# Performance work log

Hardware: AMD Instinct MI355X
Metric: run time of the kernel (lower is better)

## Reference

```python
import jax, jax.numpy as jnp
import numpy as np

KS = 16
FREQ = jnp.array([0., 1., 2., 4., 8., 16., 32., 64.], dtype=jnp.float32)  # [0]+[2^i], d=8
TWO_PI = 2.0 * np.pi


def softplus_b10(x):
    # torch F.softplus(x, beta=10, threshold=1): linear when beta*x > threshold
    bx = 10.0 * x
    return jnp.where(bx > 1.0, x, jnp.log1p(jnp.exp(jnp.minimum(bx, 1.0))) / 10.0)


def grid_sample_2d(img, gx, gy):
    # img: (C, H, W) complex; gx,gy: (N,) in [-1,1]. Bilinear, align_corners=True,
    # zero padding -- matches torch.nn.functional.grid_sample. Returns (C, N).
    C, H, W = img.shape
    ix = (gx + 1.0) * 0.5 * (W - 1)
    iy = (gy + 1.0) * 0.5 * (H - 1)
    ix0 = jnp.floor(ix)
    iy0 = jnp.floor(iy)
    wx = ix - ix0
    wy = iy - iy0

    def corner(iyc, ixc, w):
        valid = (ixc >= 0) & (ixc <= W - 1) & (iyc >= 0) & (iyc <= H - 1)
        ii = jnp.clip(ixc, 0, W - 1).astype(jnp.int32)
        jj = jnp.clip(iyc, 0, H - 1).astype(jnp.int32)
        return img[:, jj, ii] * (w * valid)[None, :]

    return (corner(iy0, ix0, (1 - wx) * (1 - wy))
            + corner(iy0, ix0 + 1, wx * (1 - wy))
            + corner(iy0 + 1, ix0, (1 - wx) * wy)
            + corner(iy0 + 1, ix0 + 1, wx * wy))


def batch_irfft(P, x):
    # P: (ks, d, N) complex; x: (N,) in [-1,1]. Trig-weighted inverse rFFT reduce.
    xx = (x + 1.0) * 0.5
    ang = TWO_PI * xx[:, None] * FREQ[None, :]            # (N, d)
    scale = jnp.where(FREQ > 0, 2.0, 1.0)
    c = jnp.cos(ang) * scale
    s = jnp.sin(ang) * scale
    return jnp.einsum('kdn,nd->kn', P.real, c) - jnp.einsum('kdn,nd->kn', P.imag, s)


def reference(xyz, bound, alpha_params, Pu_re, Pu_im, Pv_re, Pv_im, Pw_re, Pw_im):
    alpha = softplus_b10(alpha_params)[0]
    Pu = jnp.fft.ifftn((Pu_re + 1j * Pu_im) * alpha, axes=(3, 4))  # (1,ks,dx,Ny,Nz)
    Pv = jnp.fft.ifftn((Pv_re + 1j * Pv_im) * alpha, axes=(2, 4))  # (1,ks,Nx,dy,Nz)
    Pw = jnp.fft.ifftn((Pw_re + 1j * Pw_im) * alpha, axes=(2, 3))  # (1,ks,Nx,Ny,dz)

    xyzn = xyz / bound
    xs, ys, zs = xyzn[:, 0], xyzn[:, 1], xyzn[:, 2]
    N = xs.shape[0]

    ks, dx = Pu.shape[1], Pu.shape[2]
    dy = Pv.shape[3]
    dz = Pw.shape[4]

    # Pu: sample over (Ny, Nz) plane; grid (x=zs -> width Nz, y=ys -> height Ny)
    Px = grid_sample_2d(Pu[0].reshape(ks * dx, Pu.shape[3], Pu.shape[4]), zs, ys).reshape(ks, dx, N)
    # Pv: transpose (ks,Nx,dy,Nz)->(ks,dy,Nx,Nz); grid (x=zs -> Nz, y=xs -> Nx)
    Py = grid_sample_2d(jnp.swapaxes(Pv[0], 1, 2).reshape(ks * dy, Pv.shape[2], Pv.shape[4]), zs, xs).reshape(ks, dy, N)
    # Pw: transpose (ks,Nx,Ny,dz)->(ks,dz,Ny,Nx); grid (x=xs -> Nx, y=ys -> Ny)
    Pz = grid_sample_2d(jnp.swapaxes(Pw[0], 1, 3).reshape(ks * dz, Pw.shape[3], Pw.shape[2]), xs, ys).reshape(ks, dz, N)

    P = batch_irfft(Px, xs) + batch_irfft(Py, ys) + batch_irfft(Pz, zs)  # (ks, N)
    return P.T  # (N, ks)


def setup_inputs() -> dict:
    key = jax.random.key(0)
    ks = jax.random.split(key, 8)
    N = 131072
    xyz = jax.random.uniform(ks[0], (N, 3), dtype=jnp.float32, minval=-1.0, maxval=1.0)
    scale = 0.05
    return {
        'xyz': xyz,
        'bound': 1.0,
        'alpha_params': jnp.full((1,), 0.001, dtype=jnp.float32),
        'Pu_re': scale * jax.random.normal(ks[1], (1, KS, 8, 160, 160), dtype=jnp.float32),
        'Pu_im': scale * jax.random.normal(ks[2], (1, KS, 8, 160, 160), dtype=jnp.float32),
        'Pv_re': scale * jax.random.normal(ks[3], (1, KS, 160, 8, 160), dtype=jnp.float32),
        'Pv_im': scale * jax.random.normal(ks[4], (1, KS, 160, 8, 160), dtype=jnp.float32),
        'Pw_re': scale * jax.random.normal(ks[5], (1, KS, 160, 160, 8), dtype=jnp.float32),
        'Pw_im': scale * jax.random.normal(ks[6], (1, KS, 160, 160, 8), dtype=jnp.float32),
    }
```

## Files before the change

### kernel.cpp

```cpp
#include <hip/hip_runtime.h>
#include <hip/hip_bf16.h>

#define G 160
#define GM1 159
#define KD 128
#define KP 320
#define PLANE_U 3276800
#define NBUCK 4096
#define TWO_PI_F 6.28318530717958647692f

#define TSCALE 256.0f
#define TSCALE_INV 0.00390625f

typedef __attribute__((ext_vector_type(8))) short bf16x8;
typedef __attribute__((ext_vector_type(4))) float f32x4;
typedef _Float16 half2t __attribute__((ext_vector_type(2)));
typedef __fp16 fp16x2 __attribute__((ext_vector_type(2)));

__device__ __forceinline__ unsigned short f2bf(float x) {
    unsigned u = __float_as_uint(x);
    unsigned r = (u + 0x7FFFu + ((u >> 16) & 1u)) >> 16;
    return (unsigned short)r;
}
__device__ __forceinline__ unsigned int packbf(float re, float im) {
    union { __hip_bfloat162 h; unsigned int u; } cv;
    cv.h = __float22bfloat162_rn(make_float2(re, im));
    return cv.u;
}
__device__ __forceinline__ half2t cvtpk(float a, float b) {
    union { fp16x2 f; half2t h; } cv;
    cv.f = __builtin_amdgcn_cvt_pkrtz(a, b);
    return cv.h;
}
__device__ __forceinline__ unsigned int packh(float re, float im) {
    union { fp16x2 f; unsigned int u; } cv;
    cv.f = __builtin_amdgcn_cvt_pkrtz(re, im);
    return cv.u;
}
__device__ __forceinline__ half2t u2h2(unsigned int u) {
    union { unsigned int u; half2t h; } cv;
    cv.u = u;
    return cv.h;
}
__device__ __forceinline__ float fdot2h(half2t a, half2t b, float acc) {
#if __has_builtin(__builtin_amdgcn_fdot2)
    return __builtin_amdgcn_fdot2(a, b, acc, false);
#else
    return acc + (float)a.x * (float)b.x + (float)a.y * (float)b.y;
#endif
}
__device__ __forceinline__ unsigned int wim_of(unsigned int u) {
    return ((u << 16) | (u >> 16)) ^ 0x00008000u;
}
__device__ __forceinline__ unsigned part1by2(unsigned x) {
    x &= 0x3FF;
    x = (x | (x << 16)) & 0xFF0000FFu;
    x = (x | (x << 8))  & 0x0300F00Fu;
    x = (x | (x << 4))  & 0x030C30C3u;
    x = (x | (x << 2))  & 0x09249249u;
    return x;
}
__device__ __forceinline__ unsigned morton_key(float x, float y, float z) {
    int cx = min(max((int)((x + 1.0f) * 8.0f), 0), 15);
    int cy = min(max((int)((y + 1.0f) * 8.0f), 0), 15);
    int cz = min(max((int)((z + 1.0f) * 8.0f), 0), 15);
    return part1by2(cx) | (part1by2(cy) << 1) | (part1by2(cz) << 2);
}

__global__ __launch_bounds__(256) void k_prep(
    const float* __restrict__ Pw_re, const float* __restrict__ Pw_im,
    unsigned int* __restrict__ Apw, unsigned short* __restrict__ Wre,
    unsigned int* __restrict__ counts)
{
    __shared__ unsigned int sT[64 * 33];
    int b = blockIdx.x;
    int tid = threadIdx.x;
    if (b < 16) {
        counts[b * 256 + tid] = 0;
        return;
    }
    if (b < 216) {
        int idx = (b - 16) * 256 + tid;
        int r = idx / KP, kp = idx - r * KP;
        int q = kp >> 1;
        int m = (r * q) % G;
        float th = (float)m * (TWO_PI_F / (float)G);
        float s, c;
        __sincosf(th, &s, &c);
        Wre[idx] = f2bf(((kp & 1) == 0 ? c : -s) * (1.0f / (float)G));
        return;
    }
    int b2 = b - 216;
    int k  = b2 / 100;
    int rem = b2 - k * 100;
    int pc = rem / 5;
    int q0 = (rem - pc * 5) * 32;

    int i = tid & 63, qo = tid >> 6;
    size_t base = (size_t)k * 204800 + (size_t)pc * 64 + i;
    #pragma unroll
    for (int qc = 0; qc < 8; qc++) {
        int q = q0 + qo * 8 + qc;
        float r  = Pw_re[base + (size_t)q * 1280];
        float im = Pw_im[base + (size_t)q * 1280];
        sT[i * 33 + qo * 8 + qc] = packbf(r, im);
    }
    __syncthreads();
    int qp = tid & 31, mo = tid >> 5;
    #pragma unroll
    for (int mc = 0; mc < 8; mc++) {
        int m = (k * 8 + mo) * G + pc * 8 + mc;
        Apw[(size_t)m * G + q0 + qp] = sT[(mc * 8 + mo) * 33 + qp];
    }
}

__global__ __launch_bounds__(256) void k_hist(
    const float* __restrict__ xyz, const float* __restrict__ bound,
    unsigned int* __restrict__ counts, int N)
{
    int i = blockIdx.x * blockDim.x + threadIdx.x;
    if (i >= N) return;
    float invb = 1.0f / bound[0];
    float x = xyz[3 * i + 0] * invb;
    float y = xyz[3 * i + 1] * invb;
    float z = xyz[3 * i + 2] * invb;
    atomicAdd(&counts[morton_key(x, y, z)], 1u);
}

__global__ __launch_bounds__(1024) void k_scan(
    const unsigned int* __restrict__ counts,
    unsigned int* __restrict__ cursors)
{
    __shared__ unsigned int ws[16];
    int t = threadIdx.x;
    int lane = t & 63, wid = t >> 6;
    unsigned int local[4];
    unsigned int s = 0;
    #pragma unroll
    for (int i = 0; i < 4; i++) { local[i] = counts[t * 4 + i]; s += local[i]; }
    unsigned int sl = s;
    #pragma unroll
    for (int off = 1; off < 64; off <<= 1) {
        unsigned int v = __shfl_up(s, off, 64);
        if (lane >= off) s += v;
    }
    if (lane == 63) ws[wid] = s;
    __syncthreads();
    if (t < 16) {
        unsigned int x = ws[t];
        #pragma unroll
        for (int off = 1; off < 16; off <<= 1) {
            unsigned int v = __shfl_up(x, off, 64);
            if (t >= off) x += v;
        }
        ws[t] = x;
    }
    __syncthreads();
    unsigned int run = s - sl + (wid > 0 ? ws[wid - 1] : 0u);
    #pragma unroll
    for (int i = 0; i < 4; i++) { cursors[t * 4 + i] = run; run += local[i]; }
}

__global__ __launch_bounds__(256) void k_scatter(
    const float* __restrict__ xyz, const float* __restrict__ bound,
    unsigned int* __restrict__ cursors, float4* __restrict__ sxyz, int N)
{
    int i = blockIdx.x * blockDim.x + threadIdx.x;
    if (i >= N) return;
    float invb = 1.0f / bound[0];
    float x = xyz[3 * i + 0] * invb;
    float y = xyz[3 * i + 1] * invb;
    float z = xyz[3 * i + 2] * invb;
    unsigned int pos = atomicAdd(&cursors[morton_key(x, y, z)], 1u);
    sxyz[pos] = make_float4(x, y, z, __int_as_float(i));
}

__global__ __launch_bounds__(512) void k_stage1(
    const float* __restrict__ Pu_re, const float* __restrict__ Pu_im,
    const float* __restrict__ Pv_re, const float* __restrict__ Pv_im,
    const unsigned int* __restrict__ Apw,
    const float* __restrict__ alpha_params,
    const unsigned short* __restrict__ Wre,
    unsigned int* __restrict__ Bfrag)
{
    __shared__ __align__(16) unsigned short sW[51200];
    int tid = threadIdx.x;
    int w = tid >> 6, lane = tid & 63;
    int col = lane & 15, g4 = lane >> 4;
    int gw = blockIdx.x * 8 + w;
    int mt0 = gw * 2;
    int plane = mt0 / 1280;
    int mtl0 = mt0 - plane * 1280;

    for (int chunk = tid; chunk < 6400; chunk += 512) {
        int lt = chunk / 640;
        int r  = chunk - lt * 640;
        int t  = r >> 6;
        int ln = r & 63;
        int c  = ln & 15, g = ln >> 4;
        uint4 v = *(const uint4*)&Wre[(lt * 16 + c) * KP + t * 32 + g * 8];
        *(uint4*)&sW[chunk * 8] = v;
    }

    float ap = alpha_params[0];
    float bxv = 10.0f * ap;
    float alpha = (bxv > 1.0f) ? ap : log1pf(expf(fminf(bxv, 1.0f))) * 0.1f;
    alpha *= TSCALE;

    bf16x8 afr[2][10];
    #pragma unroll
    for (int ti = 0; ti < 2; ti++) {
        int mtl = mtl0 + ti;
        if (plane == 2) {
            const unsigned int* a2 = Apw + (size_t)(mtl * 16 + col) * G + g4 * 4;
            #pragma unroll
            for (int t = 0; t < 10; t++) {
                union { uint4 u; bf16x8 b; } cv;
                cv.u = *(const uint4*)(a2 + t * 16);
                afr[ti][t] = cv.b;
            }
        } else {
            const float *Ar, *Ai; int sd_, sp_;
            if (plane == 0) { Ar = Pu_re; Ai = Pu_im; sd_ = 25600; sp_ = 160; }
            else            { Ar = Pv_re; Ai = Pv_im; sd_ = 160;   sp_ = 1280; }
            int m = mtl * 16 + col;
            int k = m / 1280; int rm = m - k * 1280;
            int d = rm / 160; int p = rm - d * 160;
            size_t abase = (size_t)k * 204800 + (size_t)d * sd_ + (size_t)p * sp_ + g4 * 4;
            #pragma unroll
            for (int t = 0; t < 10; t++) {
                float4 vr = *(const float4*)(Ar + abase + t * 16);
                float4 vi = *(const float4*)(Ai + abase + t * 16);
                union { unsigned int u[4]; bf16x8 b; } cv;
                cv.u[0] = packbf(vr.x, vi.x); cv.u[1] = packbf(vr.y, vi.y);
                cv.u[2] = packbf(vr.z, vi.z); cv.u[3] = packbf(vr.w, vi.w);
                afr[ti][t] = cv.b;
            }
        }
    }

    __syncthreads();

    unsigned int* Bpl = Bfrag + (size_t)plane * PLANE_U;
    int kd0 = mtl0 / 10, pt0 = mtl0 - kd0 * 10;
    int mtl1 = mtl0 + 1;
    int kd1 = mtl1 / 10, pt1 = mtl1 - kd1 * 10;

    for (int lt2 = 0; lt2 < 5; lt2++) {
        int ltA = lt2 * 2, ltB = lt2 * 2 + 1;
        f32x4 arA0 = (f32x4)(0.f), aiA0 = (f32x4)(0.f);
        f32x4 arA1 = (f32x4)(0.f), aiA1 = (f32x4)(0.f);
        f32x4 arB0 = (f32x4)(0.f), aiB0 = (f32x4)(0.f);
        f32x4 arB1 = (f32x4)(0.f), aiB1 = (f32x4)(0.f);
        const unsigned short* wpA = &sW[(ltA * 640 + lane) * 8];
        const unsigned short* wpB = &sW[(ltB * 640 + lane) * 8];
        #pragma unroll
        for (int t = 0; t < 10; t++) {
            union { uint4 u; bf16x8 b; } crA, ciA, crB, ciB;
            crA.u = *(const uint4*)(wpA + t * 512);
            crB.u = *(const uint4*)(wpB + t * 512);
            ciA.u.x = wim_of(crA.u.x); ciA.u.y = wim_of(crA.u.y);
            ciA.u.z = wim_of(crA.u.z); ciA.u.w = wim_of(crA.u.w);
            ciB.u.x = wim_of(crB.u.x); ciB.u.y = wim_of(crB.u.y);
            ciB.u.z = wim_of(crB.u.z); ciB.u.w = wim_of(crB.u.w);
            arA0 = __builtin_amdgcn_mfma_f32_16x16x32_bf16(afr[0][t], crA.b, arA0, 0, 0, 0);
            aiA0 = __builtin_amdgcn_mfma_f32_16x16x32_bf16(afr[0][t], ciA.b, aiA0, 0, 0, 0);
            arB0 = __builtin_amdgcn_mfma_f32_16x16x32_bf16(afr[0][t], crB.b, arB0, 0, 0, 0);
            aiB0 = __builtin_amdgcn_mfma_f32_16x16x32_bf16(afr[0][t], ciB.b, aiB0, 0, 0, 0);
            arA1 = __builtin_amdgcn_mfma_f32_16x16x32_bf16(afr[1][t], crA.b, arA1, 0, 0, 0);
            aiA1 = __builtin_amdgcn_mfma_f32_16x16x32_bf16(afr[1][t], ciA.b, aiA1, 0, 0, 0);
            arB1 = __builtin_amdgcn_mfma_f32_16x16x32_bf16(afr[1][t], crB.b, arB1, 0, 0, 0);
            aiB1 = __builtin_amdgcn_mfma_f32_16x16x32_bf16(afr[1][t], ciB.b, aiB1, 0, 0, 0);
        }
        uint4 o;
        o.x = packbf(alpha * arA0[0], alpha * aiA0[0]);
        o.y = packbf(alpha * arA0[1], alpha * aiA0[1]);
        o.z = packbf(alpha * arA0[2], alpha * aiA0[2]);
        o.w = packbf(alpha * arA0[3], alpha * aiA0[3]);
        *(uint4*)(Bpl + (size_t)(kd0 * 10 + ltA) * 2560 + pt0 * 256 + lane * 4) = o;
        o.x = packbf(alpha * arB0[0], alpha * aiB0[0]);
        o.y = packbf(alpha * arB0[1], alpha * aiB0[1]);
        o.z = packbf(alpha * arB0[2], alpha * aiB0[2]);
        o.w = packbf(alpha * arB0[3], alpha * aiB0[3]);
        *(uint4*)(Bpl + (size_t)(kd0 * 10 + ltB) * 2560 + pt0 * 256 + lane * 4) = o;
        o.x = packbf(alpha * arA1[0], alpha * aiA1[0]);
        o.y = packbf(alpha * arA1[1], alpha * aiA1[1]);
        o.z = packbf(alpha * arA1[2], alpha * aiA1[2]);
        o.w = packbf(alpha * arA1[3], alpha * aiA1[3]);
        *(uint4*)(Bpl + (size_t)(kd1 * 10 + ltA) * 2560 + pt1 * 256 + lane * 4) = o;
        o.x = packbf(alpha * arB1[0], alpha * aiB1[0]);
        o.y = packbf(alpha * arB1[1], alpha * aiB1[1]);
        o.z = packbf(alpha * arB1[2], alpha * aiB1[2]);
        o.w = packbf(alpha * arB1[3], alpha * aiB1[3]);
        *(uint4*)(Bpl + (size_t)(kd1 * 10 + ltB) * 2560 + pt1 * 256 + lane * 4) = o;
    }
}

__global__ __launch_bounds__(640) void k_stage2(
    const unsigned int* __restrict__ Bfrag,
    const unsigned short* __restrict__ Wre,
    unsigned int* __restrict__ Tall)
{
    __shared__ __align__(16) unsigned int sB[20480];
    int tid = threadIdx.x;
    int w = tid >> 6, lane = tid & 63;
    int col = lane & 15, g4 = lane >> 4;
    int kdo = blockIdx.x;
    int lt  = blockIdx.y;
    int plane = blockIdx.z;

    const unsigned int* Bp = Bfrag + (size_t)plane * PLANE_U;
    #pragma unroll
    for (int i = 0; i < 8; i++) {
        uint4 v = *(const uint4*)(Bp + ((size_t)(kdo * 8 + i) * 10 + lt) * 2560 + tid * 4);
        *(uint4*)(sB + i * 2560 + tid * 4) = v;
    }

    bf16x8 wfr[10];
    const unsigned short* wp = &Wre[(w * 16 + col) * KP + g4 * 8];
    #pragma unroll
    for (int t = 0; t < 10; t++)
        wfr[t] = *(const bf16x8*)(wp + t * 32);

    __syncthreads();

    f32x4 ar[8], ai[8];
    #pragma unroll
    for (int i = 0; i < 8; i++) { ar[i] = (f32x4)(0.f); ai[i] = (f32x4)(0.f); }

    #pragma unroll
    for (int t = 0; t < 10; t++) {
        union { bf16x8 b; uint4 u; } cr, ci;
        cr.b = wfr[t];
        ci.u.x = wim_of(cr.u.x); ci.u.y = wim_of(cr.u.y);
        ci.u.z = wim_of(cr.u.z); ci.u.w = wim_of(cr.u.w);
        #pragma unroll
        for (int kq = 0; kq < 8; kq++) {
            bf16x8 bf = *(const bf16x8*)&sB[kq * 2560 + (t * 64 + lane) * 4];
            ar[kq] = __builtin_amdgcn_mfma_f32_16x16x32_bf16(cr.b, bf, ar[kq], 0, 0, 0);
            ai[kq] = __builtin_amdgcn_mfma_f32_16x16x32_bf16(ci.b, bf, ai[kq], 0, 0, 0);
        }
    }

    unsigned int* Tp = Tall + (size_t)plane * PLANE_U;
    #pragma unroll
    for (int reg = 0; reg < 4; reg++) {
        int j = w * 16 + g4 * 4 + reg;
        int l = lt * 16 + col;
        uint4 o0, o1;
        o0.x = packh(ar[0][reg], ai[0][reg]);
        o0.y = packh(ar[1][reg], ai[1][reg]);
        o0.z = packh(ar[2][reg], ai[2][reg]);
        o0.w = packh(ar[3][reg], ai[3][reg]);
        o1.x = packh(ar[4][reg], ai[4][reg]);
        o1.y = packh(ar[5][reg], ai[5][reg]);
        o1.z = packh(ar[6][reg], ai[6][reg]);
        o1.w = packh(ar[7][reg], ai[7][reg]);
        size_t ta = ((size_t)(j * G + l)) * KD + kdo * 8;
        *(uint4*)(Tp + ta)     = o0;
        *(uint4*)(Tp + ta + 4) = o1;
    }
}

__device__ __forceinline__ void plane_addr(const unsigned int* __restrict__ T,
    float gy, float gx, int k, const unsigned int** cp, float* wv)
{
    float iy = (gy + 1.0f) * (0.5f * (float)GM1);
    float ix = (gx + 1.0f) * (0.5f * (float)GM1);
    float iy0f = floorf(iy), ix0f = floorf(ix);
    float wy = iy - iy0f, wx = ix - ix0f;
    int iy0 = (int)iy0f, ix0 = (int)ix0f;
    int iy1 = min(iy0 + 1, GM1), ix1 = min(ix0 + 1, GM1);
    iy0 = max(min(iy0, GM1), 0); ix0 = max(min(ix0, GM1), 0);
    iy1 = max(iy1, 0); ix1 = max(ix1, 0);
    cp[0] = &T[(size_t)(iy0 * G + ix0) * KD + k * 8];
    cp[1] = &T[(size_t)(iy0 * G + ix1) * KD + k * 8];
    cp[2] = &T[(size_t)(iy1 * G + ix0) * KD + k * 8];
    cp[3] = &T[(size_t)(iy1 * G + ix1) * KD + k * 8];
    wv[0] = (1.f - wx) * (1.f - wy);
    wv[1] = wx * (1.f - wy);
    wv[2] = (1.f - wx) * wy;
    wv[3] = wx * wy;
}

__device__ __forceinline__ float plane_math(const uint4* va, const uint4* vb,
                                            const float* wv, float fc)
{
    float s1v, c1v;
    __sincosf(TWO_PI_F * fc, &s1v, &c1v);
    half2t tw[8];
    tw[0] = u2h2(0x00003C00u);
    float cd = c1v, sd = s1v;
    tw[1] = cvtpk(cd + cd, -(sd + sd));
    #pragma unroll
    for (int d = 2; d < 8; d++) {
        float t2 = cd + cd;
        float cn = __builtin_fmaf(t2, cd, -1.0f);
        float sn = t2 * sd;
        cd = cn; sd = sn;
        tw[d] = cvtpk(cd + cd, -(sd + sd));
    }
    const unsigned int* a0 = (const unsigned int*)&va[0];
    const unsigned int* a1 = (const unsigned int*)&va[1];
    const unsigned int* a2 = (const unsigned int*)&va[2];
    const unsigned int* a3 = (const unsigned int*)&va[3];
    const unsigned int* b0 = (const unsigned int*)&vb[0];
    const unsigned int* b1 = (const unsigned int*)&vb[1];
    const unsigned int* b2 = (const unsigned int*)&vb[2];
    const unsigned int* b3 = (const unsigned int*)&vb[3];
    float d0 = 0.f, d1 = 0.f, d2 = 0.f, d3 = 0.f;
    #pragma unroll
    for (int d = 0; d < 4; d++) {
        half2t t = tw[d];
        d0 = fdot2h(u2h2(a0[d]), t, d0);
        d1 = fdot2h(u2h2(a1[d]), t, d1);
        d2 = fdot2h(u2h2(a2[d]), t, d2);
        d3 = fdot2h(u2h2(a3[d]), t, d3);
    }
    #pragma unroll
    for (int d = 0; d < 4; d++) {
        half2t t = tw[d + 4];
        d0 = fdot2h(u2h2(b0[d]), t, d0);
        d1 = fdot2h(u2h2(b1[d]), t, d1);
        d2 = fdot2h(u2h2(b2[d]), t, d2);
        d3 = fdot2h(u2h2(b3[d]), t, d3);
    }
    float acc = wv[0] * d0;
    acc = __builtin_fmaf(wv[1], d1, acc);
    acc = __builtin_fmaf(wv[2], d2, acc);
    acc = __builtin_fmaf(wv[3], d3, acc);
    return acc;
}

__global__ __launch_bounds__(256, 3) void k_sample(
    const float4* __restrict__ sxyz,
    const unsigned int* __restrict__ Tu, const unsigned int* __restrict__ Tv,
    const unsigned int* __restrict__ Tw,
    float* __restrict__ out, int N)
{
    int tid = threadIdx.x;
    int k = tid & 15;
    int nblocks = (N + 15) / 16;
    int seg = blockIdx.x & 7;
    int segblocks = nblocks >> 3;
    int pid = (seg * segblocks + (blockIdx.x >> 3)) * 16 + (tid >> 4);
    if (pid >= N) return;

    float4 pw = sxyz[pid];
    int n = __float_as_int(pw.w);
    float x = pw.x, y = pw.y, z = pw.z;

    const unsigned int* cp[3][4];
    float wv[3][4];
    plane_addr(Tu, y, z, k, cp[0], wv[0]);
    plane_addr(Tv, x, z, k, cp[1], wv[1]);
    plane_addr(Tw, y, x, k, cp[2], wv[2]);

    uint4 va[3][4], vb[3][4];
    #pragma unroll
    for (int pl = 0; pl < 3; pl++)
        #pragma unroll
        for (int c = 0; c < 4; c++) {
            va[pl][c] = *(const uint4*)cp[pl][c];
            vb[pl][c] = *(const uint4*)(cp[pl][c] + 4);
        }

    float acc = plane_math(va[0], vb[0], wv[0], (x + 1.0f) * 0.5f)
              + plane_math(va[1], vb[1], wv[1], (y + 1.0f) * 0.5f)
              + plane_math(va[2], vb[2], wv[2], (z + 1.0f) * 0.5f);
    out[n * 16 + k] = acc * TSCALE_INV;
}

extern "C" void kernel_launch(void* const* d_in, const int* in_sizes, int n_in,
                              void* d_out, int out_size, void* d_ws, size_t ws_size,
                              hipStream_t stream) {
    const float* xyz          = (const float*)d_in[0];
    const float* bound        = (const float*)d_in[1];
    const float* alpha_params = (const float*)d_in[2];
    const float* Pu_re = (const float*)d_in[3];
    const float* Pu_im = (const float*)d_in[4];
    const float* Pv_re = (const float*)d_in[5];
    const float* Pv_im = (const float*)d_in[6];
    const float* Pw_re = (const float*)d_in[7];
    const float* Pw_im = (const float*)d_in[8];
    float* out = (float*)d_out;
    int N = in_sizes[0] / 3;

    char* ws = (char*)d_ws;
    unsigned short* Wre  = (unsigned short*)(ws);
    unsigned int*   Apw  = (unsigned int*)(ws + 102400);
    unsigned int*   Bfr  = (unsigned int*)(ws + 102400 + 13107200);
    unsigned int*   Tall = (unsigned int*)(ws + 102400 + 13107200 + 39321600);
    char*           ws2  = ws + 102400 + 13107200 + 39321600 + 39321600;
    unsigned int*   counts  = (unsigned int*)(ws2);
    unsigned int*   cursors = (unsigned int*)(ws2 + 16384);
    float4*         sxyz    = (float4*)(ws2 + 32768);
    unsigned int*   Tu   = Tall;
    unsigned int*   Tv   = Tall + (size_t)PLANE_U;
    unsigned int*   Tw   = Tall + (size_t)2 * PLANE_U;

    k_prep<<<1816, 256, 0, stream>>>(Pw_re, Pw_im, Apw, Wre, counts);
    k_hist<<<(N + 255) / 256, 256, 0, stream>>>(xyz, bound, counts, N);
    k_scan<<<1, 1024, 0, stream>>>(counts, cursors);
    k_scatter<<<(N + 255) / 256, 256, 0, stream>>>(xyz, bound, cursors, sxyz, N);
    k_stage1<<<240, 512, 0, stream>>>(Pu_re, Pu_im, Pv_re, Pv_im, Apw,
                                      alpha_params, Wre, Bfr);
    k_stage2<<<dim3(16, 10, 3), 640, 0, stream>>>(Bfr, Wre, Tall);
    k_sample<<<(N + 15) / 16, 256, 0, stream>>>(sxyz, Tu, Tv, Tw, out, N);
}
```

Before: 251.4 us.

## Split sampling kernel into three per-plane launches accumulating into output

The fused sampling kernel, which gathered from all three factor planes at once, is replaced by a templated kernel that handles one plane per launch. The three launches run in sequence, and the second and third read-modify-write the output. The intent is to keep only one plane's table (about 13 MB) hot in cache at a time and to lower register pressure so occupancy rises. The cost is two extra launches, repeated reads of the sorted coordinates, and extra read-modify-write traffic on the output.

Measured after the change: 249.0 us, median of 2. About the same (-0.9%).

```diff
diff --git a/kernel.cpp b/kernel.cpp
--- a/kernel.cpp
+++ b/kernel.cpp
@@ -432,10 +432,10 @@
     return acc;
 }
 
-__global__ __launch_bounds__(256, 3) void k_sample(
+template<int PL>
+__global__ __launch_bounds__(256) void k_sample1(
     const float4* __restrict__ sxyz,
-    const unsigned int* __restrict__ Tu, const unsigned int* __restrict__ Tv,
-    const unsigned int* __restrict__ Tw,
+    const unsigned int* __restrict__ T,
     float* __restrict__ out, int N)
 {
     int tid = threadIdx.x;
@@ -450,25 +450,25 @@
     int n = __float_as_int(pw.w);
     float x = pw.x, y = pw.y, z = pw.z;
 
-    const unsigned int* cp[3][4];
-    float wv[3][4];
-    plane_addr(Tu, y, z, k, cp[0], wv[0]);
-    plane_addr(Tv, x, z, k, cp[1], wv[1]);
-    plane_addr(Tw, y, x, k, cp[2], wv[2]);
-
-    uint4 va[3][4], vb[3][4];
-    #pragma unroll
-    for (int pl = 0; pl < 3; pl++)
-        #pragma unroll
-        for (int c = 0; c < 4; c++) {
-            va[pl][c] = *(const uint4*)cp[pl][c];
-            vb[pl][c] = *(const uint4*)(cp[pl][c] + 4);
-        }
-
-    float acc = plane_math(va[0], vb[0], wv[0], (x + 1.0f) * 0.5f)
-              + plane_math(va[1], vb[1], wv[1], (y + 1.0f) * 0.5f)
-              + plane_math(va[2], vb[2], wv[2], (z + 1.0f) * 0.5f);
-    out[n * 16 + k] = acc * TSCALE_INV;
+    float gy, gx, fc;
+    if (PL == 0)      { gy = y; gx = z; fc = (x + 1.0f) * 0.5f; }
+    else if (PL == 1) { gy = x; gx = z; fc = (y + 1.0f) * 0.5f; }
+    else              { gy = y; gx = x; fc = (z + 1.0f) * 0.5f; }
+
+    const unsigned int* cp[4];
+    float wv[4];
+    plane_addr(T, gy, gx, k, cp, wv);
+
+    uint4 va[4], vb[4];
+    #pragma unroll
+    for (int c = 0; c < 4; c++) {
+        va[c] = *(const uint4*)cp[c];
+        vb[c] = *(const uint4*)(cp[c] + 4);
+    }
+
+    float acc = plane_math(va, vb, wv, fc) * TSCALE_INV;
+    if (PL == 0) out[n * 16 + k] = acc;
+    else         out[n * 16 + k] += acc;
 }
 
 extern "C" void kernel_launch(void* const* d_in, const int* in_sizes, int n_in,
@@ -506,5 +506,8 @@
     k_stage1<<<240, 512, 0, stream>>>(Pu_re, Pu_im, Pv_re, Pv_im, Apw,
                                       alpha_params, Wre, Bfr);
     k_stage2<<<dim3(16, 10, 3), 640, 0, stream>>>(Bfr, Wre, Tall);
-    k_sample<<<(N + 15) / 16, 256, 0, stream>>>(sxyz, Tu, Tv, Tw, out, N);
-}
+    int sgrid = (N + 15) / 16;
+    k_sample1<0><<<sgrid, 256, 0, stream>>>(sxyz, Tu, out, N);
+    k_sample1<1><<<sgrid, 256, 0, stream>>>(sxyz, Tv, out, N);
+    k_sample1<2><<<sgrid, 256, 0, stream>>>(sxyz, Tw, out, N);
+}
```
